# Optimization experiments

Hardware: AMD Instinct MI355X
Metric: run time of the kernel (lower is better)

Reference implementation:

```python
import jax, jax.numpy as jnp
import numpy as np

D_MODEL = 64
N_HEAD = 8
MAX_REL = 16  # module hardcodes max_relative_position = 16
B, S = 8, 1024


def _linear_params(k, fan_in, fan_out):
    kw, kb = jax.random.split(k)
    s = 1.0 / np.sqrt(fan_in)
    W = jax.random.uniform(kw, (fan_in, fan_out), jnp.float32, -s, s)
    b = jax.random.uniform(kb, (fan_out,), jnp.float32, -s, s)
    return W, b


def setup_inputs() -> dict:
    key = jax.random.key(0)
    ks = jax.random.split(key, 10)
    Wq, bq = _linear_params(ks[0], D_MODEL, D_MODEL * N_HEAD)
    Wk, bk = _linear_params(ks[1], D_MODEL, D_MODEL * N_HEAD)
    Wv, bv = _linear_params(ks[2], D_MODEL, D_MODEL * N_HEAD)
    Wo, bo = _linear_params(ks[3], D_MODEL * N_HEAD, D_MODEL)
    Wkr, bkr = _linear_params(ks[4], D_MODEL, D_MODEL)
    Wqr, bqr = _linear_params(ks[5], D_MODEL, D_MODEL)
    p = jax.random.normal(ks[6], (2 * MAX_REL + 1, D_MODEL), jnp.float32)
    query = jax.random.normal(ks[7], (B, S, D_MODEL), jnp.float32)
    key_t = jax.random.normal(ks[8], (B, S, D_MODEL), jnp.float32)
    value = jax.random.normal(ks[9], (B, S, D_MODEL), jnp.float32)
    return dict(query=query, key=key_t, value=value,
                Wq=Wq, bq=bq, Wk=Wk, bk=bk, Wv=Wv, bv=bv,
                Wo=Wo, bo=bo, Wkr=Wkr, bkr=bkr, Wqr=Wqr, bqr=bqr, p=p)


def reference(query, key, value, Wq, bq, Wk, bk, Wv, bv, Wo, bo, Wkr, bkr, Wqr, bqr, p):
    Bsz, Sq, d = query.shape
    H = Wq.shape[1] // d  # head_dim == d_model in this module
    scale = jnp.sqrt(jnp.asarray(3 * d, jnp.float32))

    def heads(x, W, b):
        return (x @ W + b).reshape(Bsz, -1, H, d).transpose(0, 2, 1, 3)  # [B,H,S,d]

    q1 = heads(query, Wq, bq)
    k1 = heads(key, Wk, bk)
    v1 = heads(value, Wv, bv)

    # content-content term
    attn1 = jnp.einsum('bhqd,bhkd->bhqk', q1, k1)

    # relative-position terms. make_table uses clamp(dist, min=16, max=16)+16,
    # so every gather index is exactly 2*MAX_REL -> the gathered value is the
    # single column 2*MAX_REL of each table, broadcast over the last axis.
    k_r = p @ Wkr + bkr  # [2*MAX_REL+1, d]
    q_r = p @ Wqr + bqr
    attn2 = jnp.einsum('bhqd,d->bhq', q1, k_r[2 * MAX_REL])[..., None]  # [B,H,Sq,1]
    attn3 = jnp.einsum('bhkd,d->bhk', k1, q_r[2 * MAX_REL])[..., None]  # [B,H,Sk,1] (Sk==Sq)

    attn = jax.nn.softmax((attn1 + attn2 + attn3) / scale, axis=-1)
    x = jnp.einsum('bhqk,bhkd->bhqd', attn, v1)
    x = x.transpose(0, 2, 1, 3).reshape(Bsz, Sq, H * d)
    return x @ Wo + bo
```

## Files before the change

### kernel.cpp

```cpp
#include <hip/hip_runtime.h>
#include <hip/hip_bf16.h>


#define N_HEAD 8
#define BATCH  8
#define SEQ    1024
#define DMH    512
#define SC2    0.10411804386480816f

typedef __hip_bfloat16 bf16;
typedef __bf16 bf16x8 __attribute__((ext_vector_type(8)));
typedef __bf16 bf16x4 __attribute__((ext_vector_type(4)));
typedef float  f32x4  __attribute__((ext_vector_type(4)));

__global__ __launch_bounds__(256)
void init_kernel(const float* __restrict__ Wq, const float* __restrict__ Wk,
                 const float* __restrict__ Wv, const float* __restrict__ Wo,
                 const float* __restrict__ bo, float* __restrict__ out,
                 bf16* __restrict__ WqT, bf16* __restrict__ WkT,
                 bf16* __restrict__ WvT, bf16* __restrict__ WoT)
{
    const int idx = blockIdx.x * 256 + threadIdx.x;
    out[idx] = bo[idx & 63];
    if (idx < 512 * 64) {
        {
            const int k = idx >> 9, n = idx & 511;
            WqT[(size_t)n * 64 + k] = __float2bfloat16(Wq[idx]);
            WkT[(size_t)n * 64 + k] = __float2bfloat16(Wk[idx]);
            WvT[(size_t)n * 64 + k] = __float2bfloat16(Wv[idx]);
        }
        {
            const int k = idx >> 6, c = idx & 63;
            WoT[(size_t)c * 512 + k] = __float2bfloat16(Wo[idx]);
        }
    }
}

__global__ __launch_bounds__(256)
void qkv_mfma_kernel(const float* __restrict__ Xq, const float* __restrict__ Xk,
                     const float* __restrict__ Xv,
                     const bf16* __restrict__ WqT, const bf16* __restrict__ WkT,
                     const bf16* __restrict__ WvT,
                     const float* __restrict__ bq, const float* __restrict__ bk,
                     const float* __restrict__ bv,
                     bf16* __restrict__ Qh, bf16* __restrict__ Kh,
                     bf16* __restrict__ Vt)
{
    const int rt    = blockIdx.x;
    const int ct    = blockIdx.y;
    const int which = blockIdx.z;

    const float* __restrict__ X    = which == 0 ? Xq  : (which == 1 ? Xk  : Xv);
    const bf16*  __restrict__ WT   = which == 0 ? WqT : (which == 1 ? WkT : WvT);
    const float* __restrict__ bias = which == 0 ? bq  : (which == 1 ? bk  : bv);

    __shared__ __align__(16) bf16 Xs [128 * 72];
    __shared__ __align__(16) bf16 Wts[64 * 72];
    __shared__ float Bs[64];

    const int tid  = threadIdx.x;
    const int w4   = tid >> 6;
    const int lane = tid & 63;
    const int t16  = lane & 15;
    const int quad = lane >> 4;

    if (tid < 64) Bs[tid] = bias[ct * 64 + tid];
    for (int i = tid; i < 2048; i += 256) {
        const int r = i >> 4, c4 = (i & 15) << 2;
        const float4 v = *(const float4*)&X[(size_t)(rt * 128 + r) * 64 + c4];
        bf16 t[4] = {__float2bfloat16(v.x), __float2bfloat16(v.y),
                     __float2bfloat16(v.z), __float2bfloat16(v.w)};
        *(bf16x4*)&Xs[r * 72 + c4] = *(bf16x4*)t;
    }
    for (int i = tid; i < 512; i += 256) {
        const int r8 = i >> 3, c8 = (i & 7) << 3;
        *(bf16x8*)&Wts[r8 * 72 + c8] = *(const bf16x8*)&WT[(size_t)(ct * 64 + r8) * 64 + c8];
    }
    __syncthreads();

    bf16x8 bf0[4], bf1[4];
#pragma unroll
    for (int nt = 0; nt < 4; nt++) {
        bf0[nt] = *(const bf16x8*)&Wts[(nt * 16 + t16) * 72 + 0  + quad * 8];
        bf1[nt] = *(const bf16x8*)&Wts[(nt * 16 + t16) * 72 + 32 + quad * 8];
    }

    f32x4 acc[2][4];
#pragma unroll
    for (int rs = 0; rs < 2; rs++) {
        const int m = rs * 64 + w4 * 16 + t16;
        const bf16x8 af0 = *(const bf16x8*)&Xs[m * 72 + 0  + quad * 8];
        const bf16x8 af1 = *(const bf16x8*)&Xs[m * 72 + 32 + quad * 8];
#pragma unroll
        for (int nt = 0; nt < 4; nt++) {
            acc[rs][nt] = (f32x4){0.f, 0.f, 0.f, 0.f};
            acc[rs][nt] = __builtin_amdgcn_mfma_f32_16x16x32_bf16(af0, bf0[nt], acc[rs][nt], 0, 0, 0);
            acc[rs][nt] = __builtin_amdgcn_mfma_f32_16x16x32_bf16(af1, bf1[nt], acc[rs][nt], 0, 0, 0);
        }
    }

    const int b     = rt >> 3;
    const int sbase = (rt & 7) * 128;

    if (which < 2) {
        bf16* O = which == 0 ? Qh : Kh;
        const float sc = (which == 0) ? SC2 : 1.0f;
#pragma unroll
        for (int rs = 0; rs < 2; rs++)
#pragma unroll
            for (int rr = 0; rr < 4; rr++) {
                const int s = sbase + rs * 64 + w4 * 16 + quad * 4 + rr;
                bf16* dst = O + (((size_t)b * N_HEAD + ct) * SEQ + s) * 64 + t16;
#pragma unroll
                for (int nt = 0; nt < 4; nt++)
                    dst[nt * 16] = __float2bfloat16((acc[rs][nt][rr] + Bs[nt * 16 + t16]) * sc);
            }
    } else {
        __syncthreads();
        bf16* VtS = Xs;
#pragma unroll
        for (int rs = 0; rs < 2; rs++)
#pragma unroll
            for (int nt = 0; nt < 4; nt++)
#pragma unroll
                for (int rr = 0; rr < 4; rr++) {
                    const int rloc = rs * 64 + w4 * 16 + quad * 4 + rr;
                    VtS[(nt * 16 + t16) * 136 + rloc] =
                        __float2bfloat16(acc[rs][nt][rr] + Bs[nt * 16 + t16]);
                }
        __syncthreads();
        for (int i = tid; i < 1024; i += 256) {
            const int c = i >> 4, r8 = (i & 15) << 3;
            *(bf16x8*)&Vt[(((size_t)b * N_HEAD + ct) * 64 + c) * SEQ + sbase + r8] =
                *(const bf16x8*)&VtS[c * 136 + r8];
        }
    }
}

__global__ __launch_bounds__(512, 4)
void flash_attn_kernel(const bf16* __restrict__ Qh, const bf16* __restrict__ Kh,
                       const bf16* __restrict__ Vt, const bf16* __restrict__ WoT,
                       float* __restrict__ out)
{
    const int bhx  = blockIdx.x;
    const int qt   = blockIdx.y;
    const int b    = bhx >> 3;
    const int h    = bhx & 7;
    const int tid  = threadIdx.x;
    const int wave = tid >> 6;
    const int w4   = wave & 3;
    const int kh   = wave >> 2;
    const int lane = tid & 63;
    const int t16  = lane & 15;
    const int quad = lane >> 4;

    const size_t bh = (size_t)b * N_HEAD + h;
    const bf16* __restrict__ Qp  = Qh + bh * (SEQ * 64);
    const bf16* __restrict__ Kp  = Kh + bh * (SEQ * 64);
    const bf16* __restrict__ Vtp = Vt + bh * (64 * SEQ);

    __shared__ __align__(16) bf16 smem[36864];
    bf16* KsB  = smem;
    bf16* VtsB = smem + 9216;
    bf16* PsB  = smem + 18432;

    bf16x8 qf0[2], qf1[2];
#pragma unroll
    for (int rs = 0; rs < 2; rs++) {
        const int qrow = qt * 128 + rs * 64 + w4 * 16 + t16;
        qf0[rs] = *(const bf16x8*)(Qp + (size_t)qrow * 64 + 0  + quad * 8);
        qf1[rs] = *(const bf16x8*)(Qp + (size_t)qrow * 64 + 32 + quad * 8);
    }

    f32x4 Of[2][4];
    float l_i[2][4];
#pragma unroll
    for (int rs = 0; rs < 2; rs++) {
#pragma unroll
        for (int nt = 0; nt < 4; nt++) Of[rs][nt] = (f32x4){0.f, 0.f, 0.f, 0.f};
#pragma unroll
        for (int rr = 0; rr < 4; rr++) l_i[rs][rr] = 0.f;
    }

    const int r8s = tid >> 3;
    const int c8s = (tid & 7) << 3;
    bf16x8 pre[4];
#define LOAD_TILES(kt_)                                                          \
    do {                                                                         \
        pre[0] = *(const bf16x8*)&Kp [(size_t)((kt_) * 64 + r8s) * 64 + c8s];    \
        pre[1] = *(const bf16x8*)&Vtp[(size_t)r8s * SEQ + (kt_) * 64 + c8s];     \
        pre[2] = *(const bf16x8*)&Kp [(size_t)(512 + (kt_) * 64 + r8s) * 64 + c8s]; \
        pre[3] = *(const bf16x8*)&Vtp[(size_t)r8s * SEQ + 512 + (kt_) * 64 + c8s];  \
    } while (0)

    LOAD_TILES(0);

    for (int kt = 0; kt < 8; kt++) {
        *(bf16x8*)&KsB [       r8s * 72 + c8s] = pre[0];
        *(bf16x8*)&VtsB[       r8s * 72 + c8s] = pre[1];
        *(bf16x8*)&KsB [4608 + r8s * 72 + c8s] = pre[2];
        *(bf16x8*)&VtsB[4608 + r8s * 72 + c8s] = pre[3];
        __syncthreads();

        if (kt < 7) LOAD_TILES(kt + 1);

        const bf16* Ksw  = KsB  + kh * 4608;
        const bf16* Vtsw = VtsB + kh * 4608;

        f32x4 Sf[2][4];
#pragma unroll
        for (int nt = 0; nt < 4; nt++) {
            const bf16x8 kf0 = *(const bf16x8*)&Ksw[(nt * 16 + t16) * 72 + 0  + quad * 8];
            const bf16x8 kf1 = *(const bf16x8*)&Ksw[(nt * 16 + t16) * 72 + 32 + quad * 8];
#pragma unroll
            for (int rs = 0; rs < 2; rs++) {
                Sf[rs][nt] = (f32x4){0.f, 0.f, 0.f, 0.f};
                Sf[rs][nt] = __builtin_amdgcn_mfma_f32_16x16x32_bf16(qf0[rs], kf0, Sf[rs][nt], 0, 0, 0);
                Sf[rs][nt] = __builtin_amdgcn_mfma_f32_16x16x32_bf16(qf1[rs], kf1, Sf[rs][nt], 0, 0, 0);
            }
        }

        bf16x8 pf0[2], pf1[2];
#pragma unroll
        for (int rs = 0; rs < 2; rs++) {
#pragma unroll
            for (int nt = 0; nt < 4; nt++)
#pragma unroll
                for (int rr = 0; rr < 4; rr++) {
                    const float p = exp2f(Sf[rs][nt][rr]);
                    Sf[rs][nt][rr] = p;
                    l_i[rs][rr] += p;
                }
            bf16* Psw = PsB + (rs * 8 + wave) * 1152;
#pragma unroll
            for (int nt = 0; nt < 4; nt++)
#pragma unroll
                for (int rr = 0; rr < 4; rr++)
                    Psw[(quad * 4 + rr) * 72 + nt * 16 + t16] =
                        __float2bfloat16(Sf[rs][nt][rr]);
            pf0[rs] = *(const bf16x8*)&Psw[t16 * 72 + 0  + quad * 8];
            pf1[rs] = *(const bf16x8*)&Psw[t16 * 72 + 32 + quad * 8];
        }

#pragma unroll
        for (int nt = 0; nt < 4; nt++) {
            const bf16x8 vf0 = *(const bf16x8*)&Vtsw[(nt * 16 + t16) * 72 + 0  + quad * 8];
            const bf16x8 vf1 = *(const bf16x8*)&Vtsw[(nt * 16 + t16) * 72 + 32 + quad * 8];
#pragma unroll
            for (int rs = 0; rs < 2; rs++) {
                Of[rs][nt] = __builtin_amdgcn_mfma_f32_16x16x32_bf16(pf0[rs], vf0, Of[rs][nt], 0, 0, 0);
                Of[rs][nt] = __builtin_amdgcn_mfma_f32_16x16x32_bf16(pf1[rs], vf1, Of[rs][nt], 0, 0, 0);
            }
        }
        __syncthreads();
    }
#undef LOAD_TILES

    float* Xch = (float*)smem;
    float* Lch = (float*)(smem + 17408);
    bf16*  WoS = smem + 22528;
    bf16*  Pe  = smem + 27136;

    if (kh == 1) {
#pragma unroll
        for (int rs = 0; rs < 2; rs++) {
#pragma unroll
            for (int nt = 0; nt < 4; nt++)
#pragma unroll
                for (int rr = 0; rr < 4; rr++)
                    Xch[((w4 * 2 + rs) * 64 + lane) * 17 + nt * 4 + rr] = Of[rs][nt][rr];
#pragma unroll
            for (int rr = 0; rr < 4; rr++)
                Lch[((w4 * 2 + rs) * 64 + lane) * 5 + rr] = l_i[rs][rr];
        }
    }
    {
        const int r8 = tid >> 3, c8 = (tid & 7) << 3;
        *(bf16x8*)&WoS[r8 * 72 + c8] = *(const bf16x8*)&WoT[(size_t)r8 * 512 + h * 64 + c8];
    }
    __syncthreads();

    if (kh == 0) {
#pragma unroll
        for (int rs = 0; rs < 2; rs++) {
#pragma unroll
            for (int nt = 0; nt < 4; nt++)
#pragma unroll
                for (int rr = 0; rr < 4; rr++)
                    Of[rs][nt][rr] += Xch[((w4 * 2 + rs) * 64 + lane) * 17 + nt * 4 + rr];
#pragma unroll
            for (int rr = 0; rr < 4; rr++)
                l_i[rs][rr] += Lch[((w4 * 2 + rs) * 64 + lane) * 5 + rr];
        }

#pragma unroll
        for (int rs = 0; rs < 2; rs++)
#pragma unroll
            for (int off = 8; off >= 1; off >>= 1)
#pragma unroll
                for (int rr = 0; rr < 4; rr++)
                    l_i[rs][rr] += __shfl_xor(l_i[rs][rr], off, 64);

        bf16* Pew = Pe + w4 * 1152;
#pragma unroll
        for (int rs = 0; rs < 2; rs++) {
            float inv_l[4];
#pragma unroll
            for (int rr = 0; rr < 4; rr++) inv_l[rr] = 1.0f / l_i[rs][rr];
#pragma unroll
            for (int nt = 0; nt < 4; nt++)
#pragma unroll
                for (int rr = 0; rr < 4; rr++)
                    Pew[(quad * 4 + rr) * 72 + nt * 16 + t16] =
                        __float2bfloat16(Of[rs][nt][rr] * inv_l[rr]);

            const bf16x8 pf0 = *(const bf16x8*)&Pew[t16 * 72 + 0  + quad * 8];
            const bf16x8 pf1 = *(const bf16x8*)&Pew[t16 * 72 + 32 + quad * 8];

            f32x4 R[4];
#pragma unroll
            for (int nt = 0; nt < 4; nt++) {
                R[nt] = (f32x4){0.f, 0.f, 0.f, 0.f};
                const bf16x8 wf0 = *(const bf16x8*)&WoS[(nt * 16 + t16) * 72 + 0  + quad * 8];
                const bf16x8 wf1 = *(const bf16x8*)&WoS[(nt * 16 + t16) * 72 + 32 + quad * 8];
                R[nt] = __builtin_amdgcn_mfma_f32_16x16x32_bf16(pf0, wf0, R[nt], 0, 0, 0);
                R[nt] = __builtin_amdgcn_mfma_f32_16x16x32_bf16(pf1, wf1, R[nt], 0, 0, 0);
            }

            const int srow_base = qt * 128 + rs * 64 + w4 * 16 + quad * 4;
#pragma unroll
            for (int rr = 0; rr < 4; rr++) {
                const size_t base = ((size_t)b * SEQ + srow_base + rr) * 64;
#pragma unroll
                for (int nt = 0; nt < 4; nt++)
                    atomicAdd(&out[base + nt * 16 + t16], R[nt][rr]);
            }
        }
    }
}

extern "C" void kernel_launch(void* const* d_in, const int* in_sizes, int n_in,
                              void* d_out, int out_size, void* d_ws, size_t ws_size,
                              hipStream_t stream)
{
    const float* query = (const float*)d_in[0];
    const float* key_  = (const float*)d_in[1];
    const float* value = (const float*)d_in[2];
    const float* Wq    = (const float*)d_in[3];
    const float* bq    = (const float*)d_in[4];
    const float* Wk    = (const float*)d_in[5];
    const float* bk    = (const float*)d_in[6];
    const float* Wv    = (const float*)d_in[7];
    const float* bv    = (const float*)d_in[8];
    const float* Wo    = (const float*)d_in[9];
    const float* bo    = (const float*)d_in[10];

    float* out = (float*)d_out;
    char* ws   = (char*)d_ws;
    bf16* Qh  = (bf16*)(ws + (size_t) 0 * 1024 * 1024);
    bf16* Kh  = (bf16*)(ws + (size_t) 8 * 1024 * 1024);
    bf16* Vt  = (bf16*)(ws + (size_t)16 * 1024 * 1024);
    bf16* WoT = (bf16*)(ws + (size_t)24 * 1024 * 1024);
    bf16* WqT = (bf16*)(ws + (size_t)24 * 1024 * 1024 + 65536);
    bf16* WkT = (bf16*)(ws + (size_t)24 * 1024 * 1024 + 131072);
    bf16* WvT = (bf16*)(ws + (size_t)24 * 1024 * 1024 + 196608);

    init_kernel<<<dim3(2048), 256, 0, stream>>>(Wq, Wk, Wv, Wo, bo, out,
                                                WqT, WkT, WvT, WoT);
    qkv_mfma_kernel<<<dim3(64, 8, 3), 256, 0, stream>>>(
        query, key_, value, WqT, WkT, WvT, bq, bk, bv, Qh, Kh, Vt);
    flash_attn_kernel<<<dim3(64, 8), 512, 0, stream>>>(Qh, Kh, Vt, WoT, out);
}
```

Before: 141.0 us.

## Fold weight transposes into consumers, stage Q/K stores, transpose score MFMA

The separate weight transpose/bf16 conversion is removed from the init kernel. Each consumer now reads fp32 weights directly and transposes them into LDS, and the init kernel writes the bias with float4 stores. Q/K projections are staged through LDS so global stores are 16-byte coalesced. In the attention loop the score MFMA operands are swapped so each lane holds a transposed P fragment it can write with one vector store, and the row-sum reduction is simplified to two shuffles. The trade-off is redundant weight conversion per block and uncoalesced scalar LDS writes in the transposes.

```diff
diff --git a/kernel.cpp b/kernel.cpp
--- a/kernel.cpp
+++ b/kernel.cpp
@@ -3,9 +3,7 @@
 
 
 #define N_HEAD 8
-#define BATCH  8
 #define SEQ    1024
-#define DMH    512
 #define SC2    0.10411804386480816f
 
 typedef __hip_bfloat16 bf16;
@@ -14,33 +12,17 @@
 typedef float  f32x4  __attribute__((ext_vector_type(4)));
 
 __global__ __launch_bounds__(256)
-void init_kernel(const float* __restrict__ Wq, const float* __restrict__ Wk,
-                 const float* __restrict__ Wv, const float* __restrict__ Wo,
-                 const float* __restrict__ bo, float* __restrict__ out,
-                 bf16* __restrict__ WqT, bf16* __restrict__ WkT,
-                 bf16* __restrict__ WvT, bf16* __restrict__ WoT)
+void init_kernel(const float* __restrict__ bo, float* __restrict__ out)
 {
     const int idx = blockIdx.x * 256 + threadIdx.x;
-    out[idx] = bo[idx & 63];
-    if (idx < 512 * 64) {
-        {
-            const int k = idx >> 9, n = idx & 511;
-            WqT[(size_t)n * 64 + k] = __float2bfloat16(Wq[idx]);
-            WkT[(size_t)n * 64 + k] = __float2bfloat16(Wk[idx]);
-            WvT[(size_t)n * 64 + k] = __float2bfloat16(Wv[idx]);
-        }
-        {
-            const int k = idx >> 6, c = idx & 63;
-            WoT[(size_t)c * 512 + k] = __float2bfloat16(Wo[idx]);
-        }
-    }
+    *(float4*)&out[(size_t)idx << 2] = *(const float4*)&bo[(idx & 15) << 2];
 }
 
 __global__ __launch_bounds__(256)
 void qkv_mfma_kernel(const float* __restrict__ Xq, const float* __restrict__ Xk,
                      const float* __restrict__ Xv,
-                     const bf16* __restrict__ WqT, const bf16* __restrict__ WkT,
-                     const bf16* __restrict__ WvT,
+                     const float* __restrict__ Wq, const float* __restrict__ Wk,
+                     const float* __restrict__ Wv,
                      const float* __restrict__ bq, const float* __restrict__ bk,
                      const float* __restrict__ bv,
                      bf16* __restrict__ Qh, bf16* __restrict__ Kh,
@@ -50,9 +32,9 @@
     const int ct    = blockIdx.y;
     const int which = blockIdx.z;
 
-    const float* __restrict__ X    = which == 0 ? Xq  : (which == 1 ? Xk  : Xv);
-    const bf16*  __restrict__ WT   = which == 0 ? WqT : (which == 1 ? WkT : WvT);
-    const float* __restrict__ bias = which == 0 ? bq  : (which == 1 ? bk  : bv);
+    const float* __restrict__ X    = which == 0 ? Xq : (which == 1 ? Xk : Xv);
+    const float* __restrict__ W    = which == 0 ? Wq : (which == 1 ? Wk : Wv);
+    const float* __restrict__ bias = which == 0 ? bq : (which == 1 ? bk : bv);
 
     __shared__ __align__(16) bf16 Xs [128 * 72];
     __shared__ __align__(16) bf16 Wts[64 * 72];
@@ -72,9 +54,13 @@
                      __float2bfloat16(v.z), __float2bfloat16(v.w)};
         *(bf16x4*)&Xs[r * 72 + c4] = *(bf16x4*)t;
     }
-    for (int i = tid; i < 512; i += 256) {
-        const int r8 = i >> 3, c8 = (i & 7) << 3;
-        *(bf16x8*)&Wts[r8 * 72 + c8] = *(const bf16x8*)&WT[(size_t)(ct * 64 + r8) * 64 + c8];
+    for (int i = tid; i < 1024; i += 256) {
+        const int k = i >> 4, n4 = (i & 15) << 2;
+        const float4 w = *(const float4*)&W[(size_t)k * 512 + ct * 64 + n4];
+        Wts[(n4 + 0) * 72 + k] = __float2bfloat16(w.x);
+        Wts[(n4 + 1) * 72 + k] = __float2bfloat16(w.y);
+        Wts[(n4 + 2) * 72 + k] = __float2bfloat16(w.z);
+        Wts[(n4 + 3) * 72 + k] = __float2bfloat16(w.w);
     }
     __syncthreads();
 
@@ -102,21 +88,29 @@
     const int b     = rt >> 3;
     const int sbase = (rt & 7) * 128;
 
+    __syncthreads();
+
     if (which < 2) {
+        bf16* Cs = Xs;
+        const float sc = (which == 0) ? SC2 : 1.0f;
+#pragma unroll
+        for (int rs = 0; rs < 2; rs++)
+#pragma unroll
+            for (int nt = 0; nt < 4; nt++)
+#pragma unroll
+                for (int rr = 0; rr < 4; rr++) {
+                    const int row = rs * 64 + w4 * 16 + quad * 4 + rr;
+                    Cs[row * 72 + nt * 16 + t16] =
+                        __float2bfloat16((acc[rs][nt][rr] + Bs[nt * 16 + t16]) * sc);
+                }
+        __syncthreads();
         bf16* O = which == 0 ? Qh : Kh;
-        const float sc = (which == 0) ? SC2 : 1.0f;
-#pragma unroll
-        for (int rs = 0; rs < 2; rs++)
-#pragma unroll
-            for (int rr = 0; rr < 4; rr++) {
-                const int s = sbase + rs * 64 + w4 * 16 + quad * 4 + rr;
-                bf16* dst = O + (((size_t)b * N_HEAD + ct) * SEQ + s) * 64 + t16;
-#pragma unroll
-                for (int nt = 0; nt < 4; nt++)
-                    dst[nt * 16] = __float2bfloat16((acc[rs][nt][rr] + Bs[nt * 16 + t16]) * sc);
-            }
+        for (int i = tid; i < 1024; i += 256) {
+            const int r = i >> 3, c8 = (i & 7) << 3;
+            *(bf16x8*)&O[(((size_t)b * N_HEAD + ct) * SEQ + sbase + r) * 64 + c8] =
+                *(const bf16x8*)&Cs[r * 72 + c8];
+        }
     } else {
-        __syncthreads();
         bf16* VtS = Xs;
 #pragma unroll
         for (int rs = 0; rs < 2; rs++)
@@ -139,7 +133,7 @@
 
 __global__ __launch_bounds__(512, 4)
 void flash_attn_kernel(const bf16* __restrict__ Qh, const bf16* __restrict__ Kh,
-                       const bf16* __restrict__ Vt, const bf16* __restrict__ WoT,
+                       const bf16* __restrict__ Vt, const float* __restrict__ Wo,
                        float* __restrict__ out)
 {
     const int bhx  = blockIdx.x;
@@ -215,29 +209,26 @@
 #pragma unroll
             for (int rs = 0; rs < 2; rs++) {
                 Sf[rs][nt] = (f32x4){0.f, 0.f, 0.f, 0.f};
-                Sf[rs][nt] = __builtin_amdgcn_mfma_f32_16x16x32_bf16(qf0[rs], kf0, Sf[rs][nt], 0, 0, 0);
-                Sf[rs][nt] = __builtin_amdgcn_mfma_f32_16x16x32_bf16(qf1[rs], kf1, Sf[rs][nt], 0, 0, 0);
+                Sf[rs][nt] = __builtin_amdgcn_mfma_f32_16x16x32_bf16(kf0, qf0[rs], Sf[rs][nt], 0, 0, 0);
+                Sf[rs][nt] = __builtin_amdgcn_mfma_f32_16x16x32_bf16(kf1, qf1[rs], Sf[rs][nt], 0, 0, 0);
             }
         }
 
         bf16x8 pf0[2], pf1[2];
 #pragma unroll
         for (int rs = 0; rs < 2; rs++) {
-#pragma unroll
-            for (int nt = 0; nt < 4; nt++)
+            bf16* Psw = PsB + (rs * 8 + wave) * 1152;
+#pragma unroll
+            for (int nt = 0; nt < 4; nt++) {
+                bf16 pkt[4];
 #pragma unroll
                 for (int rr = 0; rr < 4; rr++) {
                     const float p = exp2f(Sf[rs][nt][rr]);
-                    Sf[rs][nt][rr] = p;
                     l_i[rs][rr] += p;
+                    pkt[rr] = __float2bfloat16(p);
                 }
-            bf16* Psw = PsB + (rs * 8 + wave) * 1152;
-#pragma unroll
-            for (int nt = 0; nt < 4; nt++)
-#pragma unroll
-                for (int rr = 0; rr < 4; rr++)
-                    Psw[(quad * 4 + rr) * 72 + nt * 16 + t16] =
-                        __float2bfloat16(Sf[rs][nt][rr]);
+                *(bf16x4*)&Psw[t16 * 72 + nt * 16 + quad * 4] = *(bf16x4*)pkt;
+            }
             pf0[rs] = *(const bf16x8*)&Psw[t16 * 72 + 0  + quad * 8];
             pf1[rs] = *(const bf16x8*)&Psw[t16 * 72 + 32 + quad * 8];
         }
@@ -256,10 +247,18 @@
     }
 #undef LOAD_TILES
 
+    float L[2];
+#pragma unroll
+    for (int rs = 0; rs < 2; rs++) {
+        L[rs] = (l_i[rs][0] + l_i[rs][1]) + (l_i[rs][2] + l_i[rs][3]);
+        L[rs] += __shfl_xor(L[rs], 16, 64);
+        L[rs] += __shfl_xor(L[rs], 32, 64);
+    }
+
     float* Xch = (float*)smem;
     float* Lch = (float*)(smem + 17408);
-    bf16*  WoS = smem + 22528;
-    bf16*  Pe  = smem + 27136;
+    bf16*  WoS = smem + 18432;
+    bf16*  Pe  = smem + 23040;
 
     if (kh == 1) {
 #pragma unroll
@@ -269,14 +268,14 @@
 #pragma unroll
                 for (int rr = 0; rr < 4; rr++)
                     Xch[((w4 * 2 + rs) * 64 + lane) * 17 + nt * 4 + rr] = Of[rs][nt][rr];
-#pragma unroll
-            for (int rr = 0; rr < 4; rr++)
-                Lch[((w4 * 2 + rs) * 64 + lane) * 5 + rr] = l_i[rs][rr];
+            Lch[(w4 * 2 + rs) * 64 + lane] = L[rs];
         }
     }
     {
-        const int r8 = tid >> 3, c8 = (tid & 7) << 3;
-        *(bf16x8*)&WoS[r8 * 72 + c8] = *(const bf16x8*)&WoT[(size_t)r8 * 512 + h * 64 + c8];
+        for (int i = tid; i < 4096; i += 512) {
+            const int kk = i >> 6, c = i & 63;
+            WoS[c * 72 + kk] = __float2bfloat16(Wo[(size_t)(h * 64 + kk) * 64 + c]);
+        }
     }
     __syncthreads();
 
@@ -288,25 +287,16 @@
 #pragma unroll
                 for (int rr = 0; rr < 4; rr++)
                     Of[rs][nt][rr] += Xch[((w4 * 2 + rs) * 64 + lane) * 17 + nt * 4 + rr];
-#pragma unroll
-            for (int rr = 0; rr < 4; rr++)
-                l_i[rs][rr] += Lch[((w4 * 2 + rs) * 64 + lane) * 5 + rr];
-        }
-
-#pragma unroll
-        for (int rs = 0; rs < 2; rs++)
-#pragma unroll
-            for (int off = 8; off >= 1; off >>= 1)
-#pragma unroll
-                for (int rr = 0; rr < 4; rr++)
-                    l_i[rs][rr] += __shfl_xor(l_i[rs][rr], off, 64);
+            L[rs] += Lch[(w4 * 2 + rs) * 64 + lane];
+        }
 
         bf16* Pew = Pe + w4 * 1152;
 #pragma unroll
         for (int rs = 0; rs < 2; rs++) {
+            const float inv = 1.0f / L[rs];
             float inv_l[4];
 #pragma unroll
-            for (int rr = 0; rr < 4; rr++) inv_l[rr] = 1.0f / l_i[rs][rr];
+            for (int rr = 0; rr < 4; rr++) inv_l[rr] = __shfl(inv, quad * 4 + rr, 64);
 #pragma unroll
             for (int nt = 0; nt < 4; nt++)
 #pragma unroll
@@ -357,17 +347,12 @@
 
     float* out = (float*)d_out;
     char* ws   = (char*)d_ws;
-    bf16* Qh  = (bf16*)(ws + (size_t) 0 * 1024 * 1024);
-    bf16* Kh  = (bf16*)(ws + (size_t) 8 * 1024 * 1024);
-    bf16* Vt  = (bf16*)(ws + (size_t)16 * 1024 * 1024);
-    bf16* WoT = (bf16*)(ws + (size_t)24 * 1024 * 1024);
-    bf16* WqT = (bf16*)(ws + (size_t)24 * 1024 * 1024 + 65536);
-    bf16* WkT = (bf16*)(ws + (size_t)24 * 1024 * 1024 + 131072);
-    bf16* WvT = (bf16*)(ws + (size_t)24 * 1024 * 1024 + 196608);
-
-    init_kernel<<<dim3(2048), 256, 0, stream>>>(Wq, Wk, Wv, Wo, bo, out,
-                                                WqT, WkT, WvT, WoT);
+    bf16* Qh = (bf16*)(ws + (size_t) 0 * 1024 * 1024);
+    bf16* Kh = (bf16*)(ws + (size_t) 8 * 1024 * 1024);
+    bf16* Vt = (bf16*)(ws + (size_t)16 * 1024 * 1024);
+
+    init_kernel<<<dim3(512), 256, 0, stream>>>(bo, out);
     qkv_mfma_kernel<<<dim3(64, 8, 3), 256, 0, stream>>>(
-        query, key_, value, WqT, WkT, WvT, bq, bk, bv, Qh, Kh, Vt);
-    flash_attn_kernel<<<dim3(64, 8), 512, 0, stream>>>(Qh, Kh, Vt, WoT, out);
+        query, key_, value, Wq, Wk, Wv, bq, bk, bv, Qh, Kh, Vt);
+    flash_attn_kernel<<<dim3(64, 8), 512, 0, stream>>>(Qh, Kh, Vt, Wo, out);
 }
```

New measurement: 138.8 us. About the same (-1.6%).
